# Kernel tuning notes

Hardware: AMD Instinct MI355X
Metric: run time of the kernel (lower is better)

The kernel has to match this reference:

```python
import jax, jax.numpy as jnp
import numpy as np

ALPHA = 1.702
LIMIT = 7.0
TOP_K = 2
B, S, H, E, I = 2, 1024, 768, 8, 768


def setup_inputs() -> dict:
    key = jax.random.key(0)
    ks = jax.random.split(key, 7)
    scale = 0.02
    return {
        "hidden_states": jax.random.normal(ks[0], (B, S, H), dtype=jnp.float32),
        "Wr": jax.random.normal(ks[1], (H, E), dtype=jnp.float32) * scale,
        "br": jax.random.normal(ks[2], (E,), dtype=jnp.float32) * scale,
        "Wgu": jax.random.normal(ks[3], (E, H, 2 * I), dtype=jnp.float32) * scale,
        "bgu": jax.random.normal(ks[4], (E, 2 * I), dtype=jnp.float32) * scale,
        "Wd": jax.random.normal(ks[5], (E, I, H), dtype=jnp.float32) * scale,
        "bd": jax.random.normal(ks[6], (E, H), dtype=jnp.float32) * scale,
    }


def reference(hidden_states, Wr, br, Wgu, bgu, Wd, bd):
    # Router: top-K experts per token, softmax over the K selected logits
    logits = jnp.einsum("bsh,he->bse", hidden_states, Wr) + br
    topk_vals, topk_idx = jax.lax.top_k(logits, TOP_K)        # [B,S,K]
    router_scores = jax.nn.softmax(topk_vals, axis=-1)         # [B,S,K]

    # Dense-over-experts grouped GEMM (sparse_matmul reference: unselected
    # experts are computed but never read by the combine gather below).
    gu = jnp.einsum("bsh,ehf->bsef", hidden_states, Wgu) + bgu  # [B,S,E,2I]
    gu = jnp.minimum(gu, LIMIT)
    gate = gu[..., :I]
    up = jnp.maximum(gu[..., I:], -LIMIT)
    glu = gate * jax.nn.sigmoid(gate * ALPHA)
    activated = (up + 1.0) * glu                                # [B,S,E,I]

    down = jnp.einsum("bsei,eih->bseh", activated, Wd) + bd     # [B,S,E,H]

    # all_to_all_combine (num_devices=1): gather this token's K expert outputs
    sel = jnp.take_along_axis(down, topk_idx[..., None], axis=2)  # [B,S,K,H]
    output = jnp.sum(sel * router_scores[..., None], axis=2)      # [B,S,H]
    return output
```

## Files before the change

### kernel.cpp

```cpp
#include <hip/hip_runtime.h>
#include <hip/hip_bf16.h>
#include <cmath>

#define ALPHA 1.702f
#define LIMIT 7.0f

constexpr int B = 2, S = 1024, H = 768, E = 8, I = 768;
constexpr int T = B * S;
constexpr int TWO_I = 2 * I;
constexpr int CAP = T;
constexpr int NT1 = I / 64;
constexpr int NT2 = H / 64;
constexpr int MT = CAP / 128;

constexpr int RTR_BLKS = 64;
constexpr int WGU_TILES = E * (TWO_I / 64) * (H / 64);
constexpr int WD_TILES  = E * (H / 64) * (H / 64);
constexpr int PRE_BLKS = RTR_BLKS + WGU_TILES;
constexpr int G1_BLKS = MT * E * NT1;
constexpr int K1_BLKS = G1_BLKS + WD_TILES;
constexpr int G2_BLKS = MT * E * NT2;
constexpr int RED_BLKS = (T * H / 4) / 256;

typedef __attribute__((ext_vector_type(8))) short short8;
typedef __attribute__((ext_vector_type(4))) float floatx4;

__device__ __forceinline__ unsigned short f2bf(float v) {
  __hip_bfloat16 h = __float2bfloat16(v);
  return *reinterpret_cast<unsigned short*>(&h);
}

__device__ __forceinline__ void g2l16(const void* g, void* l) {
  __builtin_amdgcn_global_load_lds(
      (const __attribute__((address_space(1))) void*)g,
      (__attribute__((address_space(3))) void*)l, 16, 0, 0);
}

__device__ __forceinline__ void transpose_tile(
    const float* __restrict__ in, unsigned short* __restrict__ outw,
    int N, int n0, int k0, float (*tile)[65], int tid) {
  constexpr int K = 768;
  int jr = tid & 15, r0 = tid >> 4;
#pragma unroll
  for (int p = 0; p < 4; p++) {
    int k = r0 + p * 16;
    float4 v = *(const float4*)(in + (size_t)(k0 + k) * N + n0 + jr * 4);
    tile[k][jr * 4 + 0] = v.x;
    tile[k][jr * 4 + 1] = v.y;
    tile[k][jr * 4 + 2] = v.z;
    tile[k][jr * 4 + 3] = v.w;
  }
  __syncthreads();
#pragma unroll
  for (int p = 0; p < 4; p++) {
    int n = r0 + p * 16;
    ushort4 o;
    o.x = f2bf(tile[jr * 4 + 0][n]);
    o.y = f2bf(tile[jr * 4 + 1][n]);
    o.z = f2bf(tile[jr * 4 + 2][n]);
    o.w = f2bf(tile[jr * 4 + 3][n]);
    *(ushort4*)(outw + (size_t)(n0 + n) * K + k0 + jr * 4) = o;
  }
}

__global__ __launch_bounds__(256) void pre_router_wgu(
    const float* __restrict__ x, const float* __restrict__ Wr,
    const float* __restrict__ br, const float* __restrict__ Wgu,
    unsigned short* __restrict__ Wgt, unsigned short* __restrict__ xb,
    int* __restrict__ e_cnt, int* __restrict__ row_token,
    float* __restrict__ row_w) {
  int bid = blockIdx.x;
  int tid = threadIdx.x;

  if (bid < RTR_BLKS) {
    __shared__ int cnt_s[E];
    __shared__ int base_s[E];
    __shared__ int tok_e[E][64];
    __shared__ float wv_e[E][64];

    if (tid < E) cnt_s[tid] = 0;
    __syncthreads();

    int wave = tid >> 6;
    int lane = tid & 63;

    for (int tt = 0; tt < 8; tt++) {
      int t = bid * 32 + wave * 8 + tt;
      const float* xr = x + (size_t)t * H;

      float acc[E];
#pragma unroll
      for (int e = 0; e < E; e++) acc[e] = 0.0f;

#pragma unroll
      for (int it = 0; it < 3; it++) {
        int h4 = it * 64 + lane;
        float4 xv = *(const float4*)(xr + (size_t)h4 * 4);
        ushort4 xo;
        xo.x = f2bf(xv.x);
        xo.y = f2bf(xv.y);
        xo.z = f2bf(xv.z);
        xo.w = f2bf(xv.w);
        *(ushort4*)(xb + (size_t)t * H + (size_t)h4 * 4) = xo;
        const float* wrow = Wr + (size_t)h4 * 4 * E;
        float xs[4] = {xv.x, xv.y, xv.z, xv.w};
#pragma unroll
        for (int j = 0; j < 4; j++)
#pragma unroll
          for (int e = 0; e < E; e++) acc[e] += xs[j] * wrow[j * E + e];
      }
#pragma unroll
      for (int e = 0; e < E; e++) {
        float v = acc[e];
        for (int off = 32; off > 0; off >>= 1) v += __shfl_down(v, off, 64);
        acc[e] = v;
      }
      if (lane == 0) {
        float logits[E];
#pragma unroll
        for (int e = 0; e < E; e++) logits[e] = acc[e] + br[e];
        int i0 = 0;
        float v0 = logits[0];
#pragma unroll
        for (int e = 1; e < E; e++)
          if (logits[e] > v0) { v0 = logits[e]; i0 = e; }
        int i1 = -1;
        float v1 = -INFINITY;
#pragma unroll
        for (int e = 0; e < E; e++) {
          if (e == i0) continue;
          if (logits[e] > v1) { v1 = logits[e]; i1 = e; }
        }
        float s1 = __expf(v1 - v0);
        float denom = 1.0f + s1;
        int p0 = atomicAdd(&cnt_s[i0], 1);
        tok_e[i0][p0] = t * 2 + 0;
        wv_e[i0][p0] = 1.0f / denom;
        int p1 = atomicAdd(&cnt_s[i1], 1);
        tok_e[i1][p1] = t * 2 + 1;
        wv_e[i1][p1] = s1 / denom;
      }
    }
    __syncthreads();
    if (tid < E) base_s[tid] = atomicAdd(&e_cnt[tid], cnt_s[tid]);
    __syncthreads();
#pragma unroll
    for (int e = 0; e < E; e++) {
      int c = cnt_s[e], b0 = base_s[e];
      for (int j = tid; j < c; j += 256) {
        row_token[e * CAP + b0 + j] = tok_e[e][j];
        row_w[e * CAP + b0 + j] = wv_e[e][j];
      }
    }
    return;
  }

  __shared__ float tile[64][65];
  int q = bid - RTR_BLKS;
  int e = q / 288, rem = q % 288;
  int n0 = (rem % 24) * 64;
  int k0 = (rem / 24) * 64;
  transpose_tile(Wgu + (size_t)e * H * TWO_I, Wgt + (size_t)e * TWO_I * H,
                 TWO_I, n0, k0, tile, tid);
}

struct G1Smem {
  short As[2][128 * 64];
  short Bg[2][64 * 64];
  short Bu[2][64 * 64];
  int tok[128];
};
struct TSmem {
  float tile[64][65];
};

__global__ __launch_bounds__(256) void gemm_gu_wdT(
    const unsigned short* __restrict__ xb, const unsigned short* __restrict__ Wgt,
    const float* __restrict__ bgu, const int* __restrict__ e_cnt,
    const int* __restrict__ row_token, unsigned short* __restrict__ act,
    const float* __restrict__ Wd, unsigned short* __restrict__ Wdt) {
  __shared__ __align__(16) char smem_raw[sizeof(G1Smem)];
  int bid = blockIdx.x;
  int tid = threadIdx.x;

  if (bid >= G1_BLKS) {
    TSmem* ts = (TSmem*)smem_raw;
    int q = bid - G1_BLKS;
    int e = q / 144, rem = q % 144;
    int n0 = (rem % 12) * 64;
    int k0 = (rem / 12) * 64;
    transpose_tile(Wd + (size_t)e * H * I, Wdt + (size_t)e * H * I,
                   H, n0, k0, ts->tile, tid);
    return;
  }

  G1Smem* sm = (G1Smem*)smem_raw;
  int g = bid % (E * NT1);
  int mt = bid / (E * NT1);
  int e = g / NT1;
  int n0 = (g % NT1) * 64;
  int cnt = e_cnt[e];
  int m0 = mt * 128;
  if (m0 >= cnt) return;
  int start = e * CAP;
  const unsigned short* Wg = Wgt + (size_t)e * TWO_I * H;
  const float* bias = bgu + (size_t)e * TWO_I;

  if (tid < 128) {
    int m = m0 + tid;
    sm->tok[tid] = row_token[start + ((m < cnt) ? m : (cnt - 1))];
  }
  __syncthreads();

  int lane = tid & 63;
  int wave = tid >> 6;
  int quad = lane >> 4;
  int lrow = lane & 15;
  int wm = (wave >> 1) * 64;
  int wn = (wave & 1) * 32;

  const unsigned short* gA[4];
  int oA[4];
#pragma unroll
  for (int r = 0; r < 4; r++) {
    int s = (wave * 4 + r) * 64 + lane;
    int row = s >> 3;
    int gg = (s & 7) ^ (row & 7);
    gA[r] = xb + (size_t)(sm->tok[row] >> 1) * H + gg * 8;
    oA[r] = (wave * 4 + r) * 64 * 8;
  }
  const unsigned short *gBg[2], *gBu[2];
  int oB[2];
#pragma unroll
  for (int r = 0; r < 2; r++) {
    int s = (wave * 2 + r) * 64 + lane;
    int row = s >> 3;
    int gg = (s & 7) ^ (row & 7);
    gBg[r] = Wg + (size_t)(n0 + row) * H + gg * 8;
    gBu[r] = gBg[r] + (size_t)I * H;
    oB[r] = (wave * 2 + r) * 64 * 8;
  }

  float bgv[2], buv[2];
#pragma unroll
  for (int tj = 0; tj < 2; tj++) {
    int ncol = n0 + wn + tj * 16 + lrow;
    bgv[tj] = bias[ncol];
    buv[tj] = bias[I + ncol];
  }

  floatx4 accg[4][2], accu[4][2];
#pragma unroll
  for (int i = 0; i < 4; i++)
#pragma unroll
    for (int j = 0; j < 2; j++) {
      accg[i][j] = floatx4{0.f, 0.f, 0.f, 0.f};
      accu[i][j] = floatx4{0.f, 0.f, 0.f, 0.f};
    }

  __syncthreads();

#pragma unroll
  for (int r = 0; r < 4; r++) g2l16(gA[r], &sm->As[0][oA[r]]);
#pragma unroll
  for (int r = 0; r < 2; r++) {
    g2l16(gBg[r], &sm->Bg[0][oB[r]]);
    g2l16(gBu[r], &sm->Bu[0][oB[r]]);
  }

  constexpr int NK = H / 64;
  for (int i = 0; i < NK; i++) {
    int cb = i & 1;
    if (i + 1 < NK) {
      int nb = cb ^ 1;
      int k1 = (i + 1) * 64;
#pragma unroll
      for (int r = 0; r < 4; r++) g2l16(gA[r] + k1, &sm->As[nb][oA[r]]);
#pragma unroll
      for (int r = 0; r < 2; r++) {
        g2l16(gBg[r] + k1, &sm->Bg[nb][oB[r]]);
        g2l16(gBu[r] + k1, &sm->Bu[nb][oB[r]]);
      }
      asm volatile("s_waitcnt vmcnt(8)" ::: "memory");
    } else {
      asm volatile("s_waitcnt vmcnt(0)" ::: "memory");
    }
    __builtin_amdgcn_s_barrier();

#pragma unroll
    for (int ks = 0; ks < 2; ks++) {
      int c = ks * 4 + quad;
      short8 a[4], bg[2], bu[2];
#pragma unroll
      for (int ti = 0; ti < 4; ti++) {
        int r = wm + ti * 16 + lrow;
        a[ti] = *(const short8*)(&sm->As[cb][(r * 8 + (c ^ (r & 7))) * 8]);
      }
#pragma unroll
      for (int tj = 0; tj < 2; tj++) {
        int r = wn + tj * 16 + lrow;
        bg[tj] = *(const short8*)(&sm->Bg[cb][(r * 8 + (c ^ (r & 7))) * 8]);
        bu[tj] = *(const short8*)(&sm->Bu[cb][(r * 8 + (c ^ (r & 7))) * 8]);
      }
#pragma unroll
      for (int ti = 0; ti < 4; ti++)
#pragma unroll
        for (int tj = 0; tj < 2; tj++) {
          accg[ti][tj] = __builtin_amdgcn_mfma_f32_16x16x32_bf16(
              a[ti], bg[tj], accg[ti][tj], 0, 0, 0);
          accu[ti][tj] = __builtin_amdgcn_mfma_f32_16x16x32_bf16(
              a[ti], bu[tj], accu[ti][tj], 0, 0, 0);
        }
    }
    __builtin_amdgcn_s_barrier();
  }

#pragma unroll
  for (int ti = 0; ti < 4; ti++) {
#pragma unroll
    for (int tj = 0; tj < 2; tj++) {
      int ncol = n0 + wn + tj * 16 + lrow;
#pragma unroll
      for (int r = 0; r < 4; r++) {
        int m = m0 + wm + ti * 16 + quad * 4 + r;
        if (m < cnt) {
          float gg = accg[ti][tj][r] + bgv[tj];
          float u = accu[ti][tj][r] + buv[tj];
          gg = fminf(gg, LIMIT);
          u = fmaxf(fminf(u, LIMIT), -LIMIT);
          float glu = gg / (1.0f + __expf(-ALPHA * gg));
          act[(size_t)(start + m) * I + ncol] = f2bf((u + 1.0f) * glu);
        }
      }
    }
  }
}

__global__ __launch_bounds__(256) void gemm_down_mfma(
    const unsigned short* __restrict__ act, const unsigned short* __restrict__ Wdt,
    const float* __restrict__ bd, const int* __restrict__ e_cnt,
    const int* __restrict__ row_token, const float* __restrict__ row_w,
    float* __restrict__ down) {
  int bid = blockIdx.x;
  int g = bid % (E * NT2);
  int mt = bid / (E * NT2);
  int e = g / NT2;
  int n0 = (g % NT2) * 64;
  int cnt = e_cnt[e];
  int m0 = mt * 128;
  if (m0 >= cnt) return;
  int start = e * CAP;
  const unsigned short* Wd = Wdt + (size_t)e * H * I;
  const float* bias = bd + (size_t)e * H;

  __shared__ short As[2][128 * 64];
  __shared__ short Bs[2][64 * 64];
  __shared__ int tok[128];
  __shared__ float wts[128];

  int tid = threadIdx.x;
  if (tid < 128) {
    int m = m0 + tid;
    int mm = (m < cnt) ? m : (cnt - 1);
    tok[tid] = row_token[start + mm];
    wts[tid] = row_w[start + mm];
  }
  __syncthreads();

  int lane = tid & 63;
  int wave = tid >> 6;
  int quad = lane >> 4;
  int lrow = lane & 15;
  int wm = (wave >> 1) * 64;
  int wn = (wave & 1) * 32;

  const unsigned short* gA[4];
  int oA[4];
#pragma unroll
  for (int r = 0; r < 4; r++) {
    int s = (wave * 4 + r) * 64 + lane;
    int row = s >> 3;
    int gg = (s & 7) ^ (row & 7);
    int gm = m0 + row;
    int mm = (gm < cnt) ? gm : (cnt - 1);
    gA[r] = act + (size_t)(start + mm) * I + gg * 8;
    oA[r] = (wave * 4 + r) * 64 * 8;
  }
  const unsigned short* gB[2];
  int oB[2];
#pragma unroll
  for (int r = 0; r < 2; r++) {
    int s = (wave * 2 + r) * 64 + lane;
    int row = s >> 3;
    int gg = (s & 7) ^ (row & 7);
    gB[r] = Wd + (size_t)(n0 + row) * I + gg * 8;
    oB[r] = (wave * 2 + r) * 64 * 8;
  }

  float bdv[2];
#pragma unroll
  for (int tj = 0; tj < 2; tj++) bdv[tj] = bias[n0 + wn + tj * 16 + lrow];

  floatx4 acc[4][2];
#pragma unroll
  for (int i = 0; i < 4; i++)
#pragma unroll
    for (int j = 0; j < 2; j++) acc[i][j] = floatx4{0.f, 0.f, 0.f, 0.f};

  __syncthreads();

#pragma unroll
  for (int r = 0; r < 4; r++) g2l16(gA[r], &As[0][oA[r]]);
#pragma unroll
  for (int r = 0; r < 2; r++) g2l16(gB[r], &Bs[0][oB[r]]);

  constexpr int NK = I / 64;
  for (int i = 0; i < NK; i++) {
    int cb = i & 1;
    if (i + 1 < NK) {
      int nb = cb ^ 1;
      int k1 = (i + 1) * 64;
#pragma unroll
      for (int r = 0; r < 4; r++) g2l16(gA[r] + k1, &As[nb][oA[r]]);
#pragma unroll
      for (int r = 0; r < 2; r++) g2l16(gB[r] + k1, &Bs[nb][oB[r]]);
      asm volatile("s_waitcnt vmcnt(6)" ::: "memory");
    } else {
      asm volatile("s_waitcnt vmcnt(0)" ::: "memory");
    }
    __builtin_amdgcn_s_barrier();

#pragma unroll
    for (int ks = 0; ks < 2; ks++) {
      int c = ks * 4 + quad;
      short8 a[4], b[2];
#pragma unroll
      for (int ti = 0; ti < 4; ti++) {
        int r = wm + ti * 16 + lrow;
        a[ti] = *(const short8*)(&As[cb][(r * 8 + (c ^ (r & 7))) * 8]);
      }
#pragma unroll
      for (int tj = 0; tj < 2; tj++) {
        int r = wn + tj * 16 + lrow;
        b[tj] = *(const short8*)(&Bs[cb][(r * 8 + (c ^ (r & 7))) * 8]);
      }
#pragma unroll
      for (int ti = 0; ti < 4; ti++)
#pragma unroll
        for (int tj = 0; tj < 2; tj++)
          acc[ti][tj] = __builtin_amdgcn_mfma_f32_16x16x32_bf16(
              a[ti], b[tj], acc[ti][tj], 0, 0, 0);
    }
    __builtin_amdgcn_s_barrier();
  }

#pragma unroll
  for (int ti = 0; ti < 4; ti++) {
#pragma unroll
    for (int tj = 0; tj < 2; tj++) {
      int ncol = n0 + wn + tj * 16 + lrow;
#pragma unroll
      for (int r = 0; r < 4; r++) {
        int ml = wm + ti * 16 + quad * 4 + r;
        int m = m0 + ml;
        if (m < cnt) {
          down[(size_t)tok[ml] * H + ncol] =
              wts[ml] * (acc[ti][tj][r] + bdv[tj]);
        }
      }
    }
  }
}

__global__ __launch_bounds__(256) void reduce_out(
    const float* __restrict__ down, float* __restrict__ out) {
  int i4 = blockIdx.x * 256 + threadIdx.x;
  int t = i4 / (H / 4);
  int c = i4 % (H / 4);
  const float4* d0 = (const float4*)(down + (size_t)(2 * t) * H) + c;
  const float4* d1 = (const float4*)(down + (size_t)(2 * t + 1) * H) + c;
  float4 a = *d0, b = *d1;
  float4 r = {a.x + b.x, a.y + b.y, a.z + b.z, a.w + b.w};
  ((float4*)(out + (size_t)t * H))[c] = r;
}

extern "C" void kernel_launch(void* const* d_in, const int* in_sizes, int n_in,
                              void* d_out, int out_size, void* d_ws,
                              size_t ws_size, hipStream_t stream) {
  const float* x   = (const float*)d_in[0];
  const float* Wr  = (const float*)d_in[1];
  const float* br  = (const float*)d_in[2];
  const float* Wgu = (const float*)d_in[3];
  const float* bgu = (const float*)d_in[4];
  const float* Wd  = (const float*)d_in[5];
  const float* bd  = (const float*)d_in[6];
  float* out = (float*)d_out;

  char* w = (char*)d_ws;
  int* e_cnt = (int*)w;       w += 16 * sizeof(int);
  int* row_token = (int*)w;   w += (size_t)E * CAP * sizeof(int);
  float* row_w = (float*)w;   w += (size_t)E * CAP * sizeof(float);
  unsigned short* xb  = (unsigned short*)w; w += (size_t)T * H * 2;
  unsigned short* Wgt = (unsigned short*)w; w += (size_t)E * TWO_I * H * 2;
  unsigned short* Wdt = (unsigned short*)w; w += (size_t)E * H * I * 2;
  unsigned short* act = (unsigned short*)w; w += (size_t)E * CAP * I * 2;
  float* down = (float*)w;    w += (size_t)T * 2 * H * sizeof(float);

  hipMemsetAsync(e_cnt, 0, 16 * sizeof(int), stream);
  pre_router_wgu<<<PRE_BLKS, 256, 0, stream>>>(
      x, Wr, br, Wgu, Wgt, xb, e_cnt, row_token, row_w);
  gemm_gu_wdT<<<K1_BLKS, 256, 0, stream>>>(
      xb, Wgt, bgu, e_cnt, row_token, act, Wd, Wdt);
  gemm_down_mfma<<<G2_BLKS, 256, 0, stream>>>(
      act, Wdt, bd, e_cnt, row_token, row_w, down);
  reduce_out<<<RED_BLKS, 256, 0, stream>>>(down, out);
}
```

Baseline: 160.4 us.

## Load MFMA fragments directly from global memory, dropping LDS staging in both GEMMs

```diff
diff --git a/kernel.cpp b/kernel.cpp
--- a/kernel.cpp
+++ b/kernel.cpp
@@ -28,12 +28,6 @@
 __device__ __forceinline__ unsigned short f2bf(float v) {
   __hip_bfloat16 h = __float2bfloat16(v);
   return *reinterpret_cast<unsigned short*>(&h);
-}
-
-__device__ __forceinline__ void g2l16(const void* g, void* l) {
-  __builtin_amdgcn_global_load_lds(
-      (const __attribute__((address_space(1))) void*)g,
-      (__attribute__((address_space(3))) void*)l, 16, 0, 0);
 }
 
 __device__ __forceinline__ void transpose_tile(
@@ -164,37 +158,26 @@
                  TWO_I, n0, k0, tile, tid);
 }
 
-struct G1Smem {
-  short As[2][128 * 64];
-  short Bg[2][64 * 64];
-  short Bu[2][64 * 64];
-  int tok[128];
-};
-struct TSmem {
-  float tile[64][65];
-};
-
 __global__ __launch_bounds__(256) void gemm_gu_wdT(
     const unsigned short* __restrict__ xb, const unsigned short* __restrict__ Wgt,
     const float* __restrict__ bgu, const int* __restrict__ e_cnt,
     const int* __restrict__ row_token, unsigned short* __restrict__ act,
     const float* __restrict__ Wd, unsigned short* __restrict__ Wdt) {
-  __shared__ __align__(16) char smem_raw[sizeof(G1Smem)];
+  __shared__ float tile[64][65];
+  __shared__ int tok[128];
   int bid = blockIdx.x;
   int tid = threadIdx.x;
 
   if (bid >= G1_BLKS) {
-    TSmem* ts = (TSmem*)smem_raw;
     int q = bid - G1_BLKS;
     int e = q / 144, rem = q % 144;
     int n0 = (rem % 12) * 64;
     int k0 = (rem / 12) * 64;
     transpose_tile(Wd + (size_t)e * H * I, Wdt + (size_t)e * H * I,
-                   H, n0, k0, ts->tile, tid);
+                   H, n0, k0, tile, tid);
     return;
   }
 
-  G1Smem* sm = (G1Smem*)smem_raw;
   int g = bid % (E * NT1);
   int mt = bid / (E * NT1);
   int e = g / NT1;
@@ -208,7 +191,7 @@
 
   if (tid < 128) {
     int m = m0 + tid;
-    sm->tok[tid] = row_token[start + ((m < cnt) ? m : (cnt - 1))];
+    tok[tid] = row_token[start + ((m < cnt) ? m : (cnt - 1))];
   }
   __syncthreads();
 
@@ -219,26 +202,16 @@
   int wm = (wave >> 1) * 64;
   int wn = (wave & 1) * 32;
 
-  const unsigned short* gA[4];
-  int oA[4];
-#pragma unroll
-  for (int r = 0; r < 4; r++) {
-    int s = (wave * 4 + r) * 64 + lane;
-    int row = s >> 3;
-    int gg = (s & 7) ^ (row & 7);
-    gA[r] = xb + (size_t)(sm->tok[row] >> 1) * H + gg * 8;
-    oA[r] = (wave * 4 + r) * 64 * 8;
-  }
-  const unsigned short *gBg[2], *gBu[2];
-  int oB[2];
-#pragma unroll
-  for (int r = 0; r < 2; r++) {
-    int s = (wave * 2 + r) * 64 + lane;
-    int row = s >> 3;
-    int gg = (s & 7) ^ (row & 7);
-    gBg[r] = Wg + (size_t)(n0 + row) * H + gg * 8;
-    gBu[r] = gBg[r] + (size_t)I * H;
-    oB[r] = (wave * 2 + r) * 64 * 8;
+  const unsigned short* aP[4];
+#pragma unroll
+  for (int ti = 0; ti < 4; ti++)
+    aP[ti] = xb + (size_t)(tok[wm + ti * 16 + lrow] >> 1) * H + quad * 8;
+  const unsigned short *gP[2], *uP[2];
+#pragma unroll
+  for (int tj = 0; tj < 2; tj++) {
+    int r = n0 + wn + tj * 16 + lrow;
+    gP[tj] = Wg + (size_t)r * H + quad * 8;
+    uP[tj] = gP[tj] + (size_t)I * H;
   }
 
   float bgv[2], buv[2];
@@ -258,62 +231,39 @@
       accu[i][j] = floatx4{0.f, 0.f, 0.f, 0.f};
     }
 
-  __syncthreads();
-
-#pragma unroll
-  for (int r = 0; r < 4; r++) g2l16(gA[r], &sm->As[0][oA[r]]);
-#pragma unroll
-  for (int r = 0; r < 2; r++) {
-    g2l16(gBg[r], &sm->Bg[0][oB[r]]);
-    g2l16(gBu[r], &sm->Bu[0][oB[r]]);
-  }
-
-  constexpr int NK = H / 64;
-  for (int i = 0; i < NK; i++) {
-    int cb = i & 1;
-    if (i + 1 < NK) {
-      int nb = cb ^ 1;
-      int k1 = (i + 1) * 64;
-#pragma unroll
-      for (int r = 0; r < 4; r++) g2l16(gA[r] + k1, &sm->As[nb][oA[r]]);
-#pragma unroll
-      for (int r = 0; r < 2; r++) {
-        g2l16(gBg[r] + k1, &sm->Bg[nb][oB[r]]);
-        g2l16(gBu[r] + k1, &sm->Bu[nb][oB[r]]);
-      }
-      asm volatile("s_waitcnt vmcnt(8)" ::: "memory");
-    } else {
-      asm volatile("s_waitcnt vmcnt(0)" ::: "memory");
-    }
-    __builtin_amdgcn_s_barrier();
-
-#pragma unroll
-    for (int ks = 0; ks < 2; ks++) {
-      int c = ks * 4 + quad;
-      short8 a[4], bg[2], bu[2];
-#pragma unroll
-      for (int ti = 0; ti < 4; ti++) {
-        int r = wm + ti * 16 + lrow;
-        a[ti] = *(const short8*)(&sm->As[cb][(r * 8 + (c ^ (r & 7))) * 8]);
-      }
-#pragma unroll
-      for (int tj = 0; tj < 2; tj++) {
-        int r = wn + tj * 16 + lrow;
-        bg[tj] = *(const short8*)(&sm->Bg[cb][(r * 8 + (c ^ (r & 7))) * 8]);
-        bu[tj] = *(const short8*)(&sm->Bu[cb][(r * 8 + (c ^ (r & 7))) * 8]);
-      }
-#pragma unroll
-      for (int ti = 0; ti < 4; ti++)
-#pragma unroll
-        for (int tj = 0; tj < 2; tj++) {
-          accg[ti][tj] = __builtin_amdgcn_mfma_f32_16x16x32_bf16(
-              a[ti], bg[tj], accg[ti][tj], 0, 0, 0);
-          accu[ti][tj] = __builtin_amdgcn_mfma_f32_16x16x32_bf16(
-              a[ti], bu[tj], accu[ti][tj], 0, 0, 0);
-        }
-    }
-    __builtin_amdgcn_s_barrier();
-  }
+  constexpr int NK = H / 32;
+
+  short8 a0[4], g0[2], u0[2], a1[4], g1[2], u1[2];
+
+#define LD_FRAG(kk, A, G, U)                                         \
+  {                                                                  \
+    _Pragma("unroll") for (int ti = 0; ti < 4; ti++)                 \
+        A[ti] = *(const short8*)(aP[ti] + (kk)*32);                  \
+    _Pragma("unroll") for (int tj = 0; tj < 2; tj++) {               \
+      G[tj] = *(const short8*)(gP[tj] + (kk)*32);                    \
+      U[tj] = *(const short8*)(uP[tj] + (kk)*32);                    \
+    }                                                                \
+  }
+#define MFMA_STEP(A, G, U)                                           \
+  {                                                                  \
+    _Pragma("unroll") for (int ti = 0; ti < 4; ti++)                 \
+        _Pragma("unroll") for (int tj = 0; tj < 2; tj++) {           \
+      accg[ti][tj] = __builtin_amdgcn_mfma_f32_16x16x32_bf16(        \
+          A[ti], G[tj], accg[ti][tj], 0, 0, 0);                      \
+      accu[ti][tj] = __builtin_amdgcn_mfma_f32_16x16x32_bf16(        \
+          A[ti], U[tj], accu[ti][tj], 0, 0, 0);                      \
+    }                                                                \
+  }
+
+  LD_FRAG(0, a0, g0, u0);
+  for (int k = 0; k < NK; k += 2) {
+    LD_FRAG(k + 1, a1, g1, u1);
+    MFMA_STEP(a0, g0, u0);
+    if (k + 2 < NK) LD_FRAG(k + 2, a0, g0, u0);
+    MFMA_STEP(a1, g1, u1);
+  }
+#undef LD_FRAG
+#undef MFMA_STEP
 
 #pragma unroll
   for (int ti = 0; ti < 4; ti++) {
@@ -341,7 +291,11 @@
     const float* __restrict__ bd, const int* __restrict__ e_cnt,
     const int* __restrict__ row_token, const float* __restrict__ row_w,
     float* __restrict__ down) {
+  __shared__ int tok[128];
+  __shared__ float wts[128];
   int bid = blockIdx.x;
+  int tid = threadIdx.x;
+
   int g = bid % (E * NT2);
   int mt = bid / (E * NT2);
   int e = g / NT2;
@@ -353,12 +307,6 @@
   const unsigned short* Wd = Wdt + (size_t)e * H * I;
   const float* bias = bd + (size_t)e * H;
 
-  __shared__ short As[2][128 * 64];
-  __shared__ short Bs[2][64 * 64];
-  __shared__ int tok[128];
-  __shared__ float wts[128];
-
-  int tid = threadIdx.x;
   if (tid < 128) {
     int m = m0 + tid;
     int mm = (m < cnt) ? m : (cnt - 1);
@@ -374,27 +322,18 @@
   int wm = (wave >> 1) * 64;
   int wn = (wave & 1) * 32;
 
-  const unsigned short* gA[4];
-  int oA[4];
-#pragma unroll
-  for (int r = 0; r < 4; r++) {
-    int s = (wave * 4 + r) * 64 + lane;
-    int row = s >> 3;
-    int gg = (s & 7) ^ (row & 7);
-    int gm = m0 + row;
+  const unsigned short* aP[4];
+#pragma unroll
+  for (int ti = 0; ti < 4; ti++) {
+    int gm = m0 + wm + ti * 16 + lrow;
     int mm = (gm < cnt) ? gm : (cnt - 1);
-    gA[r] = act + (size_t)(start + mm) * I + gg * 8;
-    oA[r] = (wave * 4 + r) * 64 * 8;
-  }
-  const unsigned short* gB[2];
-  int oB[2];
-#pragma unroll
-  for (int r = 0; r < 2; r++) {
-    int s = (wave * 2 + r) * 64 + lane;
-    int row = s >> 3;
-    int gg = (s & 7) ^ (row & 7);
-    gB[r] = Wd + (size_t)(n0 + row) * I + gg * 8;
-    oB[r] = (wave * 2 + r) * 64 * 8;
+    aP[ti] = act + (size_t)(start + mm) * I + quad * 8;
+  }
+  const unsigned short* bP[2];
+#pragma unroll
+  for (int tj = 0; tj < 2; tj++) {
+    int r = n0 + wn + tj * 16 + lrow;
+    bP[tj] = Wd + (size_t)r * I + quad * 8;
   }
 
   float bdv[2];
@@ -407,52 +346,34 @@
 #pragma unroll
     for (int j = 0; j < 2; j++) acc[i][j] = floatx4{0.f, 0.f, 0.f, 0.f};
 
-  __syncthreads();
-
-#pragma unroll
-  for (int r = 0; r < 4; r++) g2l16(gA[r], &As[0][oA[r]]);
-#pragma unroll
-  for (int r = 0; r < 2; r++) g2l16(gB[r], &Bs[0][oB[r]]);
-
-  constexpr int NK = I / 64;
-  for (int i = 0; i < NK; i++) {
-    int cb = i & 1;
-    if (i + 1 < NK) {
-      int nb = cb ^ 1;
-      int k1 = (i + 1) * 64;
-#pragma unroll
-      for (int r = 0; r < 4; r++) g2l16(gA[r] + k1, &As[nb][oA[r]]);
-#pragma unroll
-      for (int r = 0; r < 2; r++) g2l16(gB[r] + k1, &Bs[nb][oB[r]]);
-      asm volatile("s_waitcnt vmcnt(6)" ::: "memory");
-    } else {
-      asm volatile("s_waitcnt vmcnt(0)" ::: "memory");
-    }
-    __builtin_amdgcn_s_barrier();
-
-#pragma unroll
-    for (int ks = 0; ks < 2; ks++) {
-      int c = ks * 4 + quad;
-      short8 a[4], b[2];
-#pragma unroll
-      for (int ti = 0; ti < 4; ti++) {
-        int r = wm + ti * 16 + lrow;
-        a[ti] = *(const short8*)(&As[cb][(r * 8 + (c ^ (r & 7))) * 8]);
-      }
-#pragma unroll
-      for (int tj = 0; tj < 2; tj++) {
-        int r = wn + tj * 16 + lrow;
-        b[tj] = *(const short8*)(&Bs[cb][(r * 8 + (c ^ (r & 7))) * 8]);
-      }
-#pragma unroll
-      for (int ti = 0; ti < 4; ti++)
-#pragma unroll
-        for (int tj = 0; tj < 2; tj++)
-          acc[ti][tj] = __builtin_amdgcn_mfma_f32_16x16x32_bf16(
-              a[ti], b[tj], acc[ti][tj], 0, 0, 0);
-    }
-    __builtin_amdgcn_s_barrier();
-  }
+  constexpr int NK = I / 32;
+
+  short8 a0[4], b0[2], a1[4], b1[2];
+
+#define LD_FRAG2(kk, A, Bv)                                          \
+  {                                                                  \
+    _Pragma("unroll") for (int ti = 0; ti < 4; ti++)                 \
+        A[ti] = *(const short8*)(aP[ti] + (kk)*32);                  \
+    _Pragma("unroll") for (int tj = 0; tj < 2; tj++)                 \
+        Bv[tj] = *(const short8*)(bP[tj] + (kk)*32);                 \
+  }
+#define MFMA_STEP2(A, Bv)                                            \
+  {                                                                  \
+    _Pragma("unroll") for (int ti = 0; ti < 4; ti++)                 \
+        _Pragma("unroll") for (int tj = 0; tj < 2; tj++)             \
+            acc[ti][tj] = __builtin_amdgcn_mfma_f32_16x16x32_bf16(   \
+                A[ti], Bv[tj], acc[ti][tj], 0, 0, 0);                \
+  }
+
+  LD_FRAG2(0, a0, b0);
+  for (int k = 0; k < NK; k += 2) {
+    LD_FRAG2(k + 1, a1, b1);
+    MFMA_STEP2(a0, b0);
+    if (k + 2 < NK) LD_FRAG2(k + 2, a0, b0);
+    MFMA_STEP2(a1, b1);
+  }
+#undef LD_FRAG2
+#undef MFMA_STEP2
 
 #pragma unroll
   for (int ti = 0; ti < 4; ti++) {
```

Measured after the change: 208.8 us. 30.2% more time.
